# Performance work log

Hardware: AMD Instinct MI355X
Metric: run time of the kernel (lower is better)

The kernel has to match this reference:

```python
import jax, jax.numpy as jnp
import numpy as np

# Model dims (match init_kwargs)
E, D, H, K = 8, 512, 1024, 2   # num_experts, input/output dim, hidden dim, top_k
B, S = 4, 2048                 # batch, seq_len


def setup_inputs() -> dict:
    key = jax.random.key(0)
    ks = jax.random.split(key, 5)
    sd = lambda fan: np.float32(1.0 / np.sqrt(fan))
    return {
        "x": jax.random.normal(ks[0], (B, S, D), jnp.float32),
        "gate_w": jax.random.normal(ks[1], (D, E), jnp.float32) * sd(D),
        "gate_b": jnp.zeros((E,), jnp.float32),
        "w1": jax.random.normal(ks[2], (E, D, H), jnp.float32) * sd(D),
        "b1": jnp.zeros((E, H), jnp.float32),
        "w2": jax.random.normal(ks[3], (E, H, D), jnp.float32) * sd(H),
        "b2": jnp.zeros((E, D), jnp.float32),
    }


def reference(x, gate_w, gate_b, w1, b1, w2, b2):
    # x: [B, S, D]
    Bb, Ss, Dd = x.shape
    xf = x.reshape(-1, Dd)                              # [N, D], N = B*S

    # Router: softmax over experts, top-k, renormalize selected weights
    logits = xf @ gate_w + gate_b                        # [N, E]
    probs = jax.nn.softmax(logits, axis=-1)              # [N, E]
    top_w, top_i = jax.lax.top_k(probs, K)               # [N, K]
    top_w = top_w / top_w.sum(axis=-1, keepdims=True)

    # Per-token combine weight for each expert (0 if not routed).
    onehot = jax.nn.one_hot(top_i, E, dtype=probs.dtype)  # [N, K, E]
    combine = jnp.einsum("nke,nk->ne", onehot, top_w)     # [N, E]

    # Expert MLPs. Dropout is inactive at inference (identity).
    # h: [E, N, H]; GELU exact (torch nn.GELU default uses erf)
    h = jax.nn.gelu(jnp.einsum("nd,edh->enh", xf, w1) + b1[:, None, :],
                    approximate=False)
    y = jnp.einsum("enh,ehd->end", h, w2) + b2[:, None, :]  # [E, N, D]

    # Weighted combine: tokens not routed to expert e have combine[:, e] == 0.
    out = jnp.einsum("end,ne->nd", y, combine).reshape(Bb, Ss, Dd)
    return out, probs.reshape(Bb, Ss, E)
```

## Files before the change

kernel.cpp:

```cpp
#include <hip/hip_runtime.h>
#include <stdint.h>

#define N_TOK 8192
#define DIM   512
#define HID   1024
#define NE    8
#define NSLOT 16384
#define MAXSLOT 17408

typedef __attribute__((ext_vector_type(8))) short short8;
typedef __attribute__((ext_vector_type(4))) float f32x4;

#define W1T_OFF  0ull
#define W2T_OFF  8388608ull
#define H_OFF    16777216ull
#define Y_OFF    52428800ull
#define XBF_OFF  52428800ull
#define TOPI_OFF 70254592ull
#define TOPW_OFF 70320128ull
#define SLOT_OFF 70385664ull
#define ROWS_OFF 70451200ull
#define RW_OFF   70520832ull
#define CNT_OFF  70590464ull

__device__ __forceinline__ unsigned int f2bfu(float f) {
  union { float f; unsigned int i; } v; v.f = f;
  unsigned int u = v.i;
  return (u + 0x7FFFu + ((u >> 16) & 1u)) >> 16;
}
__device__ __forceinline__ float bf2f(unsigned int u) {
  union { unsigned int i; float f; } v; v.i = (u & 0xFFFFu) << 16; return v.f;
}
__device__ __forceinline__ float gelu_f(float x) {
  float x2 = x * x;
  float u = x * (1.59576912f + 0.07135481f * x2);
  float ez = __expf(-u);
  return x * __builtin_amdgcn_rcpf(1.0f + ez);
}
__device__ __forceinline__ void async16(void* lds, const void* g) {
  __builtin_amdgcn_global_load_lds(
      (const __attribute__((address_space(1))) unsigned int*)g,
      (__attribute__((address_space(3))) unsigned int*)lds, 16, 0, 0);
}

__global__ __launch_bounds__(256) void k_transpose(
    const float* __restrict__ w1, const float* __restrict__ w2,
    unsigned short* __restrict__ w1t, unsigned short* __restrict__ w2t) {
  __shared__ unsigned short tile[64][68];
  int b = blockIdx.x, tid = threadIdx.x;
  const float* src; unsigned short* dst; int R, C;
  if (b < 1024) { int e = b >> 7; int t = b & 127;
    src = w1 + (size_t)e * 524288; dst = w1t + (size_t)e * 524288; R = 512; C = 1024;
    int tr = t >> 4, tc = t & 15;
    src += (size_t)tr * 64 * C + tc * 64; dst += (size_t)tc * 64 * R + tr * 64;
  } else { b -= 1024; int e = b >> 7; int t = b & 127;
    src = w2 + (size_t)e * 524288; dst = w2t + (size_t)e * 524288; R = 1024; C = 512;
    int tr = t >> 3, tc = t & 7;
    src += (size_t)tr * 64 * C + tc * 64; dst += (size_t)tc * 64 * R + tr * 64;
  }
#pragma unroll
  for (int i = 0; i < 4; ++i) {
    int l = i * 256 + tid;
    int r = l >> 4, c4 = (l & 15) << 2;
    float4 v = *(const float4*)(src + (size_t)r * C + c4);
    tile[r][c4 + 0] = (unsigned short)f2bfu(v.x);
    tile[r][c4 + 1] = (unsigned short)f2bfu(v.y);
    tile[r][c4 + 2] = (unsigned short)f2bfu(v.z);
    tile[r][c4 + 3] = (unsigned short)f2bfu(v.w);
  }
  __syncthreads();
#pragma unroll
  for (int i = 0; i < 4; ++i) {
    int l = i * 256 + tid;
    int rr = l >> 4, c4 = (l & 15) << 2;
    ushort4 v;
    v.x = tile[c4 + 0][rr]; v.y = tile[c4 + 1][rr]; v.z = tile[c4 + 2][rr]; v.w = tile[c4 + 3][rr];
    *(ushort4*)(dst + (size_t)rr * R + c4) = v;
  }
}

__global__ __launch_bounds__(256) void k_router(
    const float* __restrict__ x, const float* __restrict__ gw,
    const float* __restrict__ gb, float* __restrict__ probs_out,
    int2* __restrict__ topi, float2* __restrict__ topw,
    unsigned short* __restrict__ xbf) {
  int wave = threadIdx.x >> 6, lane = threadIdx.x & 63;
  int n = blockIdx.x * 4 + wave;
  const float4* xr = (const float4*)(x + (size_t)n * DIM);
  float4 x0 = xr[lane * 2], x1 = xr[lane * 2 + 1];
  float xf[8] = {x0.x, x0.y, x0.z, x0.w, x1.x, x1.y, x1.z, x1.w};
  uint4 pa;
  pa.x = f2bfu(xf[0]) | (f2bfu(xf[1]) << 16);
  pa.y = f2bfu(xf[2]) | (f2bfu(xf[3]) << 16);
  pa.z = f2bfu(xf[4]) | (f2bfu(xf[5]) << 16);
  pa.w = f2bfu(xf[6]) | (f2bfu(xf[7]) << 16);
  *(uint4*)(xbf + (size_t)n * DIM + lane * 8) = pa;
  float acc[8] = {0.f,0.f,0.f,0.f,0.f,0.f,0.f,0.f};
  const float4* gwr = (const float4*)gw;
#pragma unroll
  for (int j = 0; j < 8; ++j) {
    int d = lane * 8 + j;
    float4 g0 = gwr[d * 2], g1 = gwr[d * 2 + 1];
    acc[0] += xf[j] * g0.x; acc[1] += xf[j] * g0.y; acc[2] += xf[j] * g0.z; acc[3] += xf[j] * g0.w;
    acc[4] += xf[j] * g1.x; acc[5] += xf[j] * g1.y; acc[6] += xf[j] * g1.z; acc[7] += xf[j] * g1.w;
  }
#pragma unroll
  for (int o = 1; o < 64; o <<= 1)
#pragma unroll
    for (int e = 0; e < 8; ++e) acc[e] += __shfl_xor(acc[e], o, 64);
  float p[8], mx = -1e30f, s = 0.f;
#pragma unroll
  for (int e = 0; e < 8; ++e) { p[e] = acc[e] + gb[e]; mx = fmaxf(mx, p[e]); }
#pragma unroll
  for (int e = 0; e < 8; ++e) { p[e] = __expf(p[e] - mx); s += p[e]; }
  float inv = 1.f / s;
#pragma unroll
  for (int e = 0; e < 8; ++e) p[e] *= inv;
  if (lane < 8) probs_out[(size_t)n * NE + lane] = p[lane];
  if (lane == 0) {
    int i0 = 0; float v0 = p[0];
#pragma unroll
    for (int e = 1; e < 8; ++e) if (p[e] > v0) { v0 = p[e]; i0 = e; }
    int i1 = -1; float v1 = -1.f;
#pragma unroll
    for (int e = 0; e < 8; ++e) if (e != i0 && p[e] > v1) { v1 = p[e]; i1 = e; }
    float sw = 1.f / (v0 + v1);
    topi[n] = make_int2(i0, i1);
    topw[n] = make_float2(v0 * sw, v1 * sw);
  }
}

__global__ __launch_bounds__(1024) void k_count(
    const int2* __restrict__ topi, int* __restrict__ meta, int* __restrict__ chunk_base,
    int* __restrict__ rows, float* __restrict__ rw) {
  __shared__ int ch[32][8];
  __shared__ int tot[8], poff_s[9], tiles_s[8];
  int t = threadIdx.x;
  int g = t >> 5;
  if (t < 256) ((int*)ch)[t] = 0;
  __syncthreads();
  int c[8] = {0,0,0,0,0,0,0,0};
  int base_tok = t * 8;
#pragma unroll
  for (int i = 0; i < 8; ++i) {
    int2 e = topi[base_tok + i];
#pragma unroll
    for (int k = 0; k < 8; ++k) c[k] += (e.x == k) + (e.y == k);
  }
#pragma unroll
  for (int k = 0; k < 8; ++k) if (c[k]) atomicAdd(&ch[g][k], c[k]);
  __syncthreads();
  if (t < 8) {
    int a = 0;
#pragma unroll
    for (int b = 0; b < 32; ++b) { int v = ch[b][t]; ch[b][t] = a; a += v; }
    tot[t] = a; meta[t] = a;
  }
  __syncthreads();
  if (t == 0) {
    int a = 0, ts = 0;
#pragma unroll
    for (int e = 0; e < 8; ++e) {
      int tiles = (tot[e] + 127) >> 7;
      poff_s[e] = a; tiles_s[e] = tiles;
      meta[16 + e] = a; meta[32 + e] = ts;
      a += tiles << 7; ts += tiles;
    }
    poff_s[8] = a; meta[24] = a; meta[40] = ts;
  }
  __syncthreads();
  if (t < 256) {
    int b = t >> 3, e = t & 7;
    chunk_base[t] = poff_s[e] + ch[b][e];
  }
#pragma unroll
  for (int e = 0; e < 8; ++e) {
    int padn = (tiles_s[e] << 7) - tot[e];
    if (t < padn) {
      int s = poff_s[e] + tot[e] + t;
      rows[s] = 0; rw[s] = 0.f;
    }
  }
}

__global__ __launch_bounds__(256) void k_assign(
    const int2* __restrict__ topi, const float2* __restrict__ topw,
    const int* __restrict__ chunk_base,
    int* __restrict__ rows, float* __restrict__ rw, int* __restrict__ slot_of) {
  __shared__ int lcnt[8];
  __shared__ int lbase[8];
  int t = threadIdx.x, b = blockIdx.x;
  if (t < 8) { lcnt[t] = 0; lbase[t] = chunk_base[b * 8 + t]; }
  __syncthreads();
  int n = b * 256 + t;
  int2 ei = topi[n]; float2 wv = topw[n];
  int r0 = atomicAdd(&lcnt[ei.x], 1);
  int r1 = atomicAdd(&lcnt[ei.y], 1);
  int s0 = lbase[ei.x] + r0;
  int s1 = lbase[ei.y] + r1;
  rows[s0] = n; rw[s0] = wv.x; slot_of[2 * n] = s0;
  rows[s1] = n; rw[s1] = wv.y; slot_of[2 * n + 1] = s1;
}

__global__ __launch_bounds__(256) void k_gemm1(
    const unsigned short* __restrict__ xbf, const unsigned short* __restrict__ w1t,
    const float* __restrict__ b1, const int* __restrict__ meta,
    const int* __restrict__ rows, unsigned short* __restrict__ h) {
  int t = blockIdx.y;
  if (t >= meta[40]) return;
  int e = 0;
#pragma unroll
  for (int i = 1; i < 8; ++i) if (t >= meta[32 + i]) e = i;
  int mt = t - meta[32 + e];
  int row0 = meta[16 + e] + (mt << 7);
  int nt = blockIdx.x;
  __shared__ __align__(16) unsigned short As[2][8192];
  __shared__ __align__(16) unsigned short Bs[2][8192];
  int tid = threadIdx.x;
  int wave = tid >> 6, lane = tid & 63;
  int wr = wave & 1, wc = wave >> 1;
  f32x4 acc[4][4] = {};
  const unsigned short* bBase = w1t + (size_t)e * HID * DIM + (size_t)(nt * 128) * DIM;

  const unsigned short* ga[4]; const unsigned short* gb[4];
#pragma unroll
  for (int j = 0; j < 4; ++j) {
    int s = j * 256 + tid;
    int r = s >> 3;
    int cg = ((s & 7) ^ (r & 7)) << 3;
    ga[j] = xbf + (size_t)rows[row0 + r] * DIM + cg;
    gb[j] = bBase + (size_t)r * DIM + cg;
  }
  int ldst = (wave * 64) * 8;

#pragma unroll
  for (int j = 0; j < 4; ++j) {
    async16(&As[0][j * 2048 + ldst], ga[j]);
    async16(&Bs[0][j * 2048 + ldst], gb[j]);
  }
  __syncthreads();

  for (int k0 = 0; k0 < DIM; k0 += 64) {
    int cur = (k0 >> 6) & 1, nxt = cur ^ 1;
    if (k0 + 64 < DIM) {
#pragma unroll
      for (int j = 0; j < 4; ++j) {
        async16(&As[nxt][j * 2048 + ldst], ga[j] + k0 + 64);
        async16(&Bs[nxt][j * 2048 + ldst], gb[j] + k0 + 64);
      }
    }
#pragma unroll
    for (int kk = 0; kk < 2; ++kk) {
      int ca = kk * 4 + (lane >> 4);
      short8 tf[4], wf[4];
#pragma unroll
      for (int am = 0; am < 4; ++am) {
        int ra = wr * 64 + am * 16 + (lane & 15);
        tf[am] = *(const short8*)&As[cur][(ra * 8 + (ca ^ (ra & 7))) * 8];
      }
#pragma unroll
      for (int an = 0; an < 4; ++an) {
        int rb = wc * 64 + an * 16 + (lane & 15);
        wf[an] = *(const short8*)&Bs[cur][(rb * 8 + (ca ^ (rb & 7))) * 8];
      }
#pragma unroll
      for (int an = 0; an < 4; ++an)
#pragma unroll
        for (int am = 0; am < 4; ++am)
          acc[an][am] = __builtin_amdgcn_mfma_f32_16x16x32_bf16(wf[an], tf[am], acc[an][am], 0, 0, 0);
    }
    __syncthreads();
  }
  int ml = lane & 15, q = lane >> 4;
#pragma unroll
  for (int am = 0; am < 4; ++am) {
    int slot_r = row0 + wr * 64 + am * 16 + ml;
    unsigned short* hrow = h + (size_t)slot_r * HID;
#pragma unroll
    for (int an = 0; an < 4; ++an) {
      int colb = nt * 128 + wc * 64 + an * 16 + q * 4;
      float4 bias = *(const float4*)&b1[e * HID + colb];
      f32x4 v = acc[an][am];
      float g0 = gelu_f(v[0] + bias.x);
      float g1 = gelu_f(v[1] + bias.y);
      float g2 = gelu_f(v[2] + bias.z);
      float g3 = gelu_f(v[3] + bias.w);
      uint2 pk;
      pk.x = f2bfu(g0) | (f2bfu(g1) << 16);
      pk.y = f2bfu(g2) | (f2bfu(g3) << 16);
      *(uint2*)(hrow + colb) = pk;
    }
  }
}

__global__ __launch_bounds__(256) void k_gemm2(
    const unsigned short* __restrict__ h, const unsigned short* __restrict__ w2t,
    const float* __restrict__ b2, const int* __restrict__ meta,
    const float* __restrict__ rw, unsigned short* __restrict__ y) {
  int t = blockIdx.y;
  if (t >= meta[40]) return;
  int e = 0;
#pragma unroll
  for (int i = 1; i < 8; ++i) if (t >= meta[32 + i]) e = i;
  int mt = t - meta[32 + e];
  int row0 = meta[16 + e] + (mt << 7);
  int nt = blockIdx.x;
  __shared__ __align__(16) unsigned short As[2][8192];
  __shared__ __align__(16) unsigned short Bs[2][8192];
  int tid = threadIdx.x;
  int wave = tid >> 6, lane = tid & 63;
  int wr = wave & 1, wc = wave >> 1;
  f32x4 acc[4][4] = {};
  const unsigned short* aBase = h + (size_t)row0 * HID;
  const unsigned short* bBase = w2t + (size_t)e * DIM * HID + (size_t)(nt * 128) * HID;

  const unsigned short* ga[4]; const unsigned short* gb[4];
#pragma unroll
  for (int j = 0; j < 4; ++j) {
    int s = j * 256 + tid;
    int r = s >> 3;
    int cg = ((s & 7) ^ (r & 7)) << 3;
    ga[j] = aBase + (size_t)r * HID + cg;
    gb[j] = bBase + (size_t)r * HID + cg;
  }
  int ldst = (wave * 64) * 8;

#pragma unroll
  for (int j = 0; j < 4; ++j) {
    async16(&As[0][j * 2048 + ldst], ga[j]);
    async16(&Bs[0][j * 2048 + ldst], gb[j]);
  }
  __syncthreads();

  for (int k0 = 0; k0 < HID; k0 += 64) {
    int cur = (k0 >> 6) & 1, nxt = cur ^ 1;
    if (k0 + 64 < HID) {
#pragma unroll
      for (int j = 0; j < 4; ++j) {
        async16(&As[nxt][j * 2048 + ldst], ga[j] + k0 + 64);
        async16(&Bs[nxt][j * 2048 + ldst], gb[j] + k0 + 64);
      }
    }
#pragma unroll
    for (int kk = 0; kk < 2; ++kk) {
      int ca = kk * 4 + (lane >> 4);
      short8 tf[4], wf[4];
#pragma unroll
      for (int am = 0; am < 4; ++am) {
        int ra = wr * 64 + am * 16 + (lane & 15);
        tf[am] = *(const short8*)&As[cur][(ra * 8 + (ca ^ (ra & 7))) * 8];
      }
#pragma unroll
      for (int an = 0; an < 4; ++an) {
        int rb = wc * 64 + an * 16 + (lane & 15);
        wf[an] = *(const short8*)&Bs[cur][(rb * 8 + (ca ^ (rb & 7))) * 8];
      }
#pragma unroll
      for (int an = 0; an < 4; ++an)
#pragma unroll
        for (int am = 0; am < 4; ++am)
          acc[an][am] = __builtin_amdgcn_mfma_f32_16x16x32_bf16(wf[an], tf[am], acc[an][am], 0, 0, 0);
    }
    __syncthreads();
  }
  int ml = lane & 15, q = lane >> 4;
#pragma unroll
  for (int am = 0; am < 4; ++am) {
    int slot_r = row0 + wr * 64 + am * 16 + ml;
    float w = rw[slot_r];
    unsigned short* yrow = y + (size_t)slot_r * DIM;
#pragma unroll
    for (int an = 0; an < 4; ++an) {
      int colb = nt * 128 + wc * 64 + an * 16 + q * 4;
      float4 bias = *(const float4*)&b2[e * DIM + colb];
      f32x4 v = acc[an][am];
      uint2 pk;
      pk.x = f2bfu((v[0] + bias.x) * w) | (f2bfu((v[1] + bias.y) * w) << 16);
      pk.y = f2bfu((v[2] + bias.z) * w) | (f2bfu((v[3] + bias.w) * w) << 16);
      *(uint2*)(yrow + colb) = pk;
    }
  }
}

__global__ __launch_bounds__(256) void k_combine(
    const unsigned short* __restrict__ y, const int* __restrict__ slot_of,
    float* __restrict__ out) {
  int t = blockIdx.x * 256 + threadIdx.x;
  int n = t >> 6, c = (t & 63) << 3;
  int s0 = slot_of[2 * n], s1 = slot_of[2 * n + 1];
  uint4 u0 = *(const uint4*)(y + (size_t)s0 * DIM + c);
  uint4 u1 = *(const uint4*)(y + (size_t)s1 * DIM + c);
  float4 o0, o1;
  o0.x = bf2f(u0.x) + bf2f(u1.x); o0.y = bf2f(u0.x >> 16) + bf2f(u1.x >> 16);
  o0.z = bf2f(u0.y) + bf2f(u1.y); o0.w = bf2f(u0.y >> 16) + bf2f(u1.y >> 16);
  o1.x = bf2f(u0.z) + bf2f(u1.z); o1.y = bf2f(u0.z >> 16) + bf2f(u1.z >> 16);
  o1.z = bf2f(u0.w) + bf2f(u1.w); o1.w = bf2f(u0.w >> 16) + bf2f(u1.w >> 16);
  *(float4*)(out + (size_t)n * DIM + c) = o0;
  *(float4*)(out + (size_t)n * DIM + c + 4) = o1;
}

extern "C" void kernel_launch(void* const* d_in, const int* in_sizes, int n_in,
                              void* d_out, int out_size, void* d_ws, size_t ws_size,
                              hipStream_t stream) {
  const float* x  = (const float*)d_in[0];
  const float* gw = (const float*)d_in[1];
  const float* gb = (const float*)d_in[2];
  const float* w1 = (const float*)d_in[3];
  const float* b1 = (const float*)d_in[4];
  const float* w2 = (const float*)d_in[5];
  const float* b2 = (const float*)d_in[6];
  float* out = (float*)d_out;
  char* ws = (char*)d_ws;

  unsigned short* w1t = (unsigned short*)(ws + W1T_OFF);
  unsigned short* w2t = (unsigned short*)(ws + W2T_OFF);
  unsigned short* h   = (unsigned short*)(ws + H_OFF);
  unsigned short* y   = (unsigned short*)(ws + Y_OFF);
  unsigned short* xbf = (unsigned short*)(ws + XBF_OFF);
  int2*   topi    = (int2*)(ws + TOPI_OFF);
  float2* topw    = (float2*)(ws + TOPW_OFF);
  int*    slot_of = (int*)(ws + SLOT_OFF);
  int*    rows    = (int*)(ws + ROWS_OFF);
  float*  rw      = (float*)(ws + RW_OFF);
  int*    meta    = (int*)(ws + CNT_OFF);
  int*    chunk_base = meta + 64;
  float*  probs   = out + (size_t)N_TOK * DIM;

  k_transpose<<<dim3(2048), dim3(256), 0, stream>>>(w1, w2, w1t, w2t);
  k_router   <<<dim3(2048), dim3(256), 0, stream>>>(x, gw, gb, probs, topi, topw, xbf);
  k_count    <<<dim3(1),    dim3(1024), 0, stream>>>(topi, meta, chunk_base, rows, rw);
  k_assign   <<<dim3(32),   dim3(256), 0, stream>>>(topi, topw, chunk_base, rows, rw, slot_of);
  k_gemm1    <<<dim3(8, 136), dim3(256), 0, stream>>>(xbf, w1t, b1, meta, rows, h);
  k_gemm2    <<<dim3(4, 136), dim3(256), 0, stream>>>(h, w2t, b2, meta, rw, y);
  k_combine  <<<dim3(2048), dim3(256), 0, stream>>>(y, slot_of, out);
}
```

Before: 214.2 us.

## Stage GEMM tile prefetch through registers instead of direct global-to-LDS loads

Both expert GEMM kernels stop using the direct global-to-LDS async load for tiles. They now load the next tile into registers (uint4) before the MFMA loop and write those registers into the other LDS buffer afterwards, followed by a barrier. A sched_barrier keeps the compiler from moving the LDS stores ahead of the compute. The goal is to overlap global memory latency with MFMA work under explicit control. The cost is extra VGPR pressure and extra LDS store instructions, which could reduce occupancy.

Result: slower. 327.9 us (+53.1%).

```diff
diff --git a/kernel.cpp b/kernel.cpp
--- a/kernel.cpp
+++ b/kernel.cpp
@@ -36,11 +36,6 @@
   float u = x * (1.59576912f + 0.07135481f * x2);
   float ez = __expf(-u);
   return x * __builtin_amdgcn_rcpf(1.0f + ez);
-}
-__device__ __forceinline__ void async16(void* lds, const void* g) {
-  __builtin_amdgcn_global_load_lds(
-      (const __attribute__((address_space(1))) unsigned int*)g,
-      (__attribute__((address_space(3))) unsigned int*)lds, 16, 0, 0);
 }
 
 __global__ __launch_bounds__(256) void k_transpose(
@@ -222,7 +217,7 @@
   f32x4 acc[4][4] = {};
   const unsigned short* bBase = w1t + (size_t)e * HID * DIM + (size_t)(nt * 128) * DIM;
 
-  const unsigned short* ga[4]; const unsigned short* gb[4];
+  const unsigned short* ga[4]; const unsigned short* gb[4]; int lofs[4];
 #pragma unroll
   for (int j = 0; j < 4; ++j) {
     int s = j * 256 + tid;
@@ -230,23 +225,27 @@
     int cg = ((s & 7) ^ (r & 7)) << 3;
     ga[j] = xbf + (size_t)rows[row0 + r] * DIM + cg;
     gb[j] = bBase + (size_t)r * DIM + cg;
-  }
-  int ldst = (wave * 64) * 8;
-
+    lofs[j] = s * 8;
+  }
+
+  uint4 pa[4], pb[4];
+#pragma unroll
+  for (int j = 0; j < 4; ++j) { pa[j] = *(const uint4*)ga[j]; pb[j] = *(const uint4*)gb[j]; }
 #pragma unroll
   for (int j = 0; j < 4; ++j) {
-    async16(&As[0][j * 2048 + ldst], ga[j]);
-    async16(&Bs[0][j * 2048 + ldst], gb[j]);
+    *(uint4*)&As[0][lofs[j]] = pa[j];
+    *(uint4*)&Bs[0][lofs[j]] = pb[j];
   }
   __syncthreads();
 
   for (int k0 = 0; k0 < DIM; k0 += 64) {
     int cur = (k0 >> 6) & 1, nxt = cur ^ 1;
-    if (k0 + 64 < DIM) {
+    bool more = (k0 + 64 < DIM);
+    if (more) {
 #pragma unroll
       for (int j = 0; j < 4; ++j) {
-        async16(&As[nxt][j * 2048 + ldst], ga[j] + k0 + 64);
-        async16(&Bs[nxt][j * 2048 + ldst], gb[j] + k0 + 64);
+        pa[j] = *(const uint4*)(ga[j] + k0 + 64);
+        pb[j] = *(const uint4*)(gb[j] + k0 + 64);
       }
     }
 #pragma unroll
@@ -269,7 +268,15 @@
         for (int am = 0; am < 4; ++am)
           acc[an][am] = __builtin_amdgcn_mfma_f32_16x16x32_bf16(wf[an], tf[am], acc[an][am], 0, 0, 0);
     }
-    __syncthreads();
+    __builtin_amdgcn_sched_barrier(0);
+    if (more) {
+#pragma unroll
+      for (int j = 0; j < 4; ++j) {
+        *(uint4*)&As[nxt][lofs[j]] = pa[j];
+        *(uint4*)&Bs[nxt][lofs[j]] = pb[j];
+      }
+      __syncthreads();
+    }
   }
   int ml = lane & 15, q = lane >> 4;
 #pragma unroll
@@ -314,7 +321,7 @@
   const unsigned short* aBase = h + (size_t)row0 * HID;
   const unsigned short* bBase = w2t + (size_t)e * DIM * HID + (size_t)(nt * 128) * HID;
 
-  const unsigned short* ga[4]; const unsigned short* gb[4];
+  const unsigned short* ga[4]; const unsigned short* gb[4]; int lofs[4];
 #pragma unroll
   for (int j = 0; j < 4; ++j) {
     int s = j * 256 + tid;
@@ -322,23 +329,27 @@
     int cg = ((s & 7) ^ (r & 7)) << 3;
     ga[j] = aBase + (size_t)r * HID + cg;
     gb[j] = bBase + (size_t)r * HID + cg;
-  }
-  int ldst = (wave * 64) * 8;
-
+    lofs[j] = s * 8;
+  }
+
+  uint4 pa[4], pb[4];
+#pragma unroll
+  for (int j = 0; j < 4; ++j) { pa[j] = *(const uint4*)ga[j]; pb[j] = *(const uint4*)gb[j]; }
 #pragma unroll
   for (int j = 0; j < 4; ++j) {
-    async16(&As[0][j * 2048 + ldst], ga[j]);
-    async16(&Bs[0][j * 2048 + ldst], gb[j]);
+    *(uint4*)&As[0][lofs[j]] = pa[j];
+    *(uint4*)&Bs[0][lofs[j]] = pb[j];
   }
   __syncthreads();
 
   for (int k0 = 0; k0 < HID; k0 += 64) {
     int cur = (k0 >> 6) & 1, nxt = cur ^ 1;
-    if (k0 + 64 < HID) {
+    bool more = (k0 + 64 < HID);
+    if (more) {
 #pragma unroll
       for (int j = 0; j < 4; ++j) {
-        async16(&As[nxt][j * 2048 + ldst], ga[j] + k0 + 64);
-        async16(&Bs[nxt][j * 2048 + ldst], gb[j] + k0 + 64);
+        pa[j] = *(const uint4*)(ga[j] + k0 + 64);
+        pb[j] = *(const uint4*)(gb[j] + k0 + 64);
       }
     }
 #pragma unroll
@@ -361,7 +372,15 @@
         for (int am = 0; am < 4; ++am)
           acc[an][am] = __builtin_amdgcn_mfma_f32_16x16x32_bf16(wf[an], tf[am], acc[an][am], 0, 0, 0);
     }
-    __syncthreads();
+    __builtin_amdgcn_sched_barrier(0);
+    if (more) {
+#pragma unroll
+      for (int j = 0; j < 4; ++j) {
+        *(uint4*)&As[nxt][lofs[j]] = pa[j];
+        *(uint4*)&Bs[nxt][lofs[j]] = pb[j];
+      }
+      __syncthreads();
+    }
   }
   int ml = lane & 15, q = lane >> 4;
 #pragma unroll
```

## Halve GEMM K-tile to 32 with new LDS swizzle; widen transpose stores

Applied to the files above, without the earlier changes.

Both expert GEMM kernels now stage 32-wide K slices instead of 64, which halves shared memory per block (64KB to 32KB) and uses a 4-chunk XOR swizzle keyed on row pairs. The goal is higher occupancy, with more blocks resident per CU to hide latency. The cost is twice as many loop iterations and barriers, with less MFMA work per sync. The weight-transpose kernel also switches from 8-byte to 16-byte global stores.

Result: no change. 210.4 us (-1.8%).

```diff
diff --git a/kernel.cpp b/kernel.cpp
--- a/kernel.cpp
+++ b/kernel.cpp
@@ -70,12 +70,20 @@
   }
   __syncthreads();
 #pragma unroll
-  for (int i = 0; i < 4; ++i) {
+  for (int i = 0; i < 2; ++i) {
     int l = i * 256 + tid;
-    int rr = l >> 4, c4 = (l & 15) << 2;
-    ushort4 v;
-    v.x = tile[c4 + 0][rr]; v.y = tile[c4 + 1][rr]; v.z = tile[c4 + 2][rr]; v.w = tile[c4 + 3][rr];
-    *(ushort4*)(dst + (size_t)rr * R + c4) = v;
+    int rr = l >> 3, c8 = (l & 7) << 3;
+    ushort4 a, b2v;
+    a.x = tile[c8 + 0][rr]; a.y = tile[c8 + 1][rr];
+    a.z = tile[c8 + 2][rr]; a.w = tile[c8 + 3][rr];
+    b2v.x = tile[c8 + 4][rr]; b2v.y = tile[c8 + 5][rr];
+    b2v.z = tile[c8 + 6][rr]; b2v.w = tile[c8 + 7][rr];
+    uint4 pk;
+    pk.x = (unsigned int)a.x | ((unsigned int)a.y << 16);
+    pk.y = (unsigned int)a.z | ((unsigned int)a.w << 16);
+    pk.z = (unsigned int)b2v.x | ((unsigned int)b2v.y << 16);
+    pk.w = (unsigned int)b2v.z | ((unsigned int)b2v.w << 16);
+    *(uint4*)(dst + (size_t)rr * R + c8) = pk;
   }
 }
 
@@ -214,54 +222,53 @@
   int mt = t - meta[32 + e];
   int row0 = meta[16 + e] + (mt << 7);
   int nt = blockIdx.x;
-  __shared__ __align__(16) unsigned short As[2][8192];
-  __shared__ __align__(16) unsigned short Bs[2][8192];
+  __shared__ __align__(16) unsigned short As[2][4096];
+  __shared__ __align__(16) unsigned short Bs[2][4096];
   int tid = threadIdx.x;
   int wave = tid >> 6, lane = tid & 63;
   int wr = wave & 1, wc = wave >> 1;
   f32x4 acc[4][4] = {};
   const unsigned short* bBase = w1t + (size_t)e * HID * DIM + (size_t)(nt * 128) * DIM;
 
-  const unsigned short* ga[4]; const unsigned short* gb[4];
-#pragma unroll
-  for (int j = 0; j < 4; ++j) {
+  const unsigned short* ga[2]; const unsigned short* gb[2];
+#pragma unroll
+  for (int j = 0; j < 2; ++j) {
     int s = j * 256 + tid;
-    int r = s >> 3;
-    int cg = ((s & 7) ^ (r & 7)) << 3;
+    int r = s >> 2;
+    int cg = ((s & 3) ^ ((r >> 1) & 3)) << 3;
     ga[j] = xbf + (size_t)rows[row0 + r] * DIM + cg;
     gb[j] = bBase + (size_t)r * DIM + cg;
   }
   int ldst = (wave * 64) * 8;
 
 #pragma unroll
-  for (int j = 0; j < 4; ++j) {
+  for (int j = 0; j < 2; ++j) {
     async16(&As[0][j * 2048 + ldst], ga[j]);
     async16(&Bs[0][j * 2048 + ldst], gb[j]);
   }
   __syncthreads();
 
-  for (int k0 = 0; k0 < DIM; k0 += 64) {
-    int cur = (k0 >> 6) & 1, nxt = cur ^ 1;
-    if (k0 + 64 < DIM) {
-#pragma unroll
-      for (int j = 0; j < 4; ++j) {
-        async16(&As[nxt][j * 2048 + ldst], ga[j] + k0 + 64);
-        async16(&Bs[nxt][j * 2048 + ldst], gb[j] + k0 + 64);
-      }
-    }
-#pragma unroll
-    for (int kk = 0; kk < 2; ++kk) {
-      int ca = kk * 4 + (lane >> 4);
+  for (int k0 = 0; k0 < DIM; k0 += 32) {
+    int cur = (k0 >> 5) & 1, nxt = cur ^ 1;
+    if (k0 + 32 < DIM) {
+#pragma unroll
+      for (int j = 0; j < 2; ++j) {
+        async16(&As[nxt][j * 2048 + ldst], ga[j] + k0 + 32);
+        async16(&Bs[nxt][j * 2048 + ldst], gb[j] + k0 + 32);
+      }
+    }
+    {
+      int ca = lane >> 4;
       short8 tf[4], wf[4];
 #pragma unroll
       for (int am = 0; am < 4; ++am) {
         int ra = wr * 64 + am * 16 + (lane & 15);
-        tf[am] = *(const short8*)&As[cur][(ra * 8 + (ca ^ (ra & 7))) * 8];
+        tf[am] = *(const short8*)&As[cur][(ra * 4 + (ca ^ ((ra >> 1) & 3))) * 8];
       }
 #pragma unroll
       for (int an = 0; an < 4; ++an) {
         int rb = wc * 64 + an * 16 + (lane & 15);
-        wf[an] = *(const short8*)&Bs[cur][(rb * 8 + (ca ^ (rb & 7))) * 8];
+        wf[an] = *(const short8*)&Bs[cur][(rb * 4 + (ca ^ ((rb >> 1) & 3))) * 8];
       }
 #pragma unroll
       for (int an = 0; an < 4; ++an)
@@ -305,8 +312,8 @@
   int mt = t - meta[32 + e];
   int row0 = meta[16 + e] + (mt << 7);
   int nt = blockIdx.x;
-  __shared__ __align__(16) unsigned short As[2][8192];
-  __shared__ __align__(16) unsigned short Bs[2][8192];
+  __shared__ __align__(16) unsigned short As[2][4096];
+  __shared__ __align__(16) unsigned short Bs[2][4096];
   int tid = threadIdx.x;
   int wave = tid >> 6, lane = tid & 63;
   int wr = wave & 1, wc = wave >> 1;
@@ -314,46 +321,45 @@
   const unsigned short* aBase = h + (size_t)row0 * HID;
   const unsigned short* bBase = w2t + (size_t)e * DIM * HID + (size_t)(nt * 128) * HID;
 
-  const unsigned short* ga[4]; const unsigned short* gb[4];
-#pragma unroll
-  for (int j = 0; j < 4; ++j) {
+  const unsigned short* ga[2]; const unsigned short* gb[2];
+#pragma unroll
+  for (int j = 0; j < 2; ++j) {
     int s = j * 256 + tid;
-    int r = s >> 3;
-    int cg = ((s & 7) ^ (r & 7)) << 3;
+    int r = s >> 2;
+    int cg = ((s & 3) ^ ((r >> 1) & 3)) << 3;
     ga[j] = aBase + (size_t)r * HID + cg;
     gb[j] = bBase + (size_t)r * HID + cg;
   }
   int ldst = (wave * 64) * 8;
 
 #pragma unroll
-  for (int j = 0; j < 4; ++j) {
+  for (int j = 0; j < 2; ++j) {
     async16(&As[0][j * 2048 + ldst], ga[j]);
     async16(&Bs[0][j * 2048 + ldst], gb[j]);
   }
   __syncthreads();
 
-  for (int k0 = 0; k0 < HID; k0 += 64) {
-    int cur = (k0 >> 6) & 1, nxt = cur ^ 1;
-    if (k0 + 64 < HID) {
-#pragma unroll
-      for (int j = 0; j < 4; ++j) {
-        async16(&As[nxt][j * 2048 + ldst], ga[j] + k0 + 64);
-        async16(&Bs[nxt][j * 2048 + ldst], gb[j] + k0 + 64);
-      }
-    }
-#pragma unroll
-    for (int kk = 0; kk < 2; ++kk) {
-      int ca = kk * 4 + (lane >> 4);
+  for (int k0 = 0; k0 < HID; k0 += 32) {
+    int cur = (k0 >> 5) & 1, nxt = cur ^ 1;
+    if (k0 + 32 < HID) {
+#pragma unroll
+      for (int j = 0; j < 2; ++j) {
+        async16(&As[nxt][j * 2048 + ldst], ga[j] + k0 + 32);
+        async16(&Bs[nxt][j * 2048 + ldst], gb[j] + k0 + 32);
+      }
+    }
+    {
+      int ca = lane >> 4;
       short8 tf[4], wf[4];
 #pragma unroll
       for (int am = 0; am < 4; ++am) {
         int ra = wr * 64 + am * 16 + (lane & 15);
-        tf[am] = *(const short8*)&As[cur][(ra * 8 + (ca ^ (ra & 7))) * 8];
+        tf[am] = *(const short8*)&As[cur][(ra * 4 + (ca ^ ((ra >> 1) & 3))) * 8];
       }
 #pragma unroll
       for (int an = 0; an < 4; ++an) {
         int rb = wc * 64 + an * 16 + (lane & 15);
-        wf[an] = *(const short8*)&Bs[cur][(rb * 8 + (ca ^ (rb & 7))) * 8];
+        wf[an] = *(const short8*)&Bs[cur][(rb * 4 + (ca ^ ((rb >> 1) & 3))) * 8];
       }
 #pragma unroll
       for (int an = 0; an < 4; ++an)
```

## Fuse transpose with router, widen transpose stores, halve gemm2 N tile

Applied to the files above, without the earlier changes.

The weight transpose/bf16 conversion and the router are merged into one launch with 4096 blocks, removing a kernel boundary and letting the two independent jobs overlap. The transpose write-back now stores 8 bf16 values (16 bytes) per thread instead of 4. gemm2 switches from 128x128 tiles to 128x64 tiles, with each wave owning 32 rows by 64 columns, which doubles the grid to 8x136 for more parallelism. The cost is more A-tile reloads in gemm2 and less MFMA work per LDS read.

New measurement: 219.7 us. +2.6%, slower.

```diff
diff --git a/kernel.cpp b/kernel.cpp
--- a/kernel.cpp
+++ b/kernel.cpp
@@ -43,11 +43,62 @@
       (__attribute__((address_space(3))) unsigned int*)lds, 16, 0, 0);
 }
 
-__global__ __launch_bounds__(256) void k_transpose(
+__global__ __launch_bounds__(256) void k_prep(
     const float* __restrict__ w1, const float* __restrict__ w2,
-    unsigned short* __restrict__ w1t, unsigned short* __restrict__ w2t) {
+    unsigned short* __restrict__ w1t, unsigned short* __restrict__ w2t,
+    const float* __restrict__ x, const float* __restrict__ gw,
+    const float* __restrict__ gb, float* __restrict__ probs_out,
+    int2* __restrict__ topi, float2* __restrict__ topw,
+    unsigned short* __restrict__ xbf) {
   __shared__ unsigned short tile[64][68];
   int b = blockIdx.x, tid = threadIdx.x;
+  if (b >= 2048) {
+    int wave = tid >> 6, lane = tid & 63;
+    int n = (b - 2048) * 4 + wave;
+    const float4* xr = (const float4*)(x + (size_t)n * DIM);
+    float4 x0 = xr[lane * 2], x1 = xr[lane * 2 + 1];
+    float xf[8] = {x0.x, x0.y, x0.z, x0.w, x1.x, x1.y, x1.z, x1.w};
+    uint4 pa;
+    pa.x = f2bfu(xf[0]) | (f2bfu(xf[1]) << 16);
+    pa.y = f2bfu(xf[2]) | (f2bfu(xf[3]) << 16);
+    pa.z = f2bfu(xf[4]) | (f2bfu(xf[5]) << 16);
+    pa.w = f2bfu(xf[6]) | (f2bfu(xf[7]) << 16);
+    *(uint4*)(xbf + (size_t)n * DIM + lane * 8) = pa;
+    float acc[8] = {0.f,0.f,0.f,0.f,0.f,0.f,0.f,0.f};
+    const float4* gwr = (const float4*)gw;
+#pragma unroll
+    for (int j = 0; j < 8; ++j) {
+      int d = lane * 8 + j;
+      float4 g0 = gwr[d * 2], g1 = gwr[d * 2 + 1];
+      acc[0] += xf[j] * g0.x; acc[1] += xf[j] * g0.y; acc[2] += xf[j] * g0.z; acc[3] += xf[j] * g0.w;
+      acc[4] += xf[j] * g1.x; acc[5] += xf[j] * g1.y; acc[6] += xf[j] * g1.z; acc[7] += xf[j] * g1.w;
+    }
+#pragma unroll
+    for (int o = 1; o < 64; o <<= 1)
+#pragma unroll
+      for (int e = 0; e < 8; ++e) acc[e] += __shfl_xor(acc[e], o, 64);
+    float p[8], mx = -1e30f, s = 0.f;
+#pragma unroll
+    for (int e = 0; e < 8; ++e) { p[e] = acc[e] + gb[e]; mx = fmaxf(mx, p[e]); }
+#pragma unroll
+    for (int e = 0; e < 8; ++e) { p[e] = __expf(p[e] - mx); s += p[e]; }
+    float inv = 1.f / s;
+#pragma unroll
+    for (int e = 0; e < 8; ++e) p[e] *= inv;
+    if (lane < 8) probs_out[(size_t)n * NE + lane] = p[lane];
+    if (lane == 0) {
+      int i0 = 0; float v0 = p[0];
+#pragma unroll
+      for (int e = 1; e < 8; ++e) if (p[e] > v0) { v0 = p[e]; i0 = e; }
+      int i1 = -1; float v1 = -1.f;
+#pragma unroll
+      for (int e = 0; e < 8; ++e) if (e != i0 && p[e] > v1) { v1 = p[e]; i1 = e; }
+      float sw = 1.f / (v0 + v1);
+      topi[n] = make_int2(i0, i1);
+      topw[n] = make_float2(v0 * sw, v1 * sw);
+    }
+    return;
+  }
   const float* src; unsigned short* dst; int R, C;
   if (b < 1024) { int e = b >> 7; int t = b & 127;
     src = w1 + (size_t)e * 524288; dst = w1t + (size_t)e * 524288; R = 512; C = 1024;
@@ -70,63 +121,20 @@
   }
   __syncthreads();
 #pragma unroll
-  for (int i = 0; i < 4; ++i) {
+  for (int i = 0; i < 2; ++i) {
     int l = i * 256 + tid;
-    int rr = l >> 4, c4 = (l & 15) << 2;
-    ushort4 v;
-    v.x = tile[c4 + 0][rr]; v.y = tile[c4 + 1][rr]; v.z = tile[c4 + 2][rr]; v.w = tile[c4 + 3][rr];
-    *(ushort4*)(dst + (size_t)rr * R + c4) = v;
-  }
-}
-
-__global__ __launch_bounds__(256) void k_router(
-    const float* __restrict__ x, const float* __restrict__ gw,
-    const float* __restrict__ gb, float* __restrict__ probs_out,
-    int2* __restrict__ topi, float2* __restrict__ topw,
-    unsigned short* __restrict__ xbf) {
-  int wave = threadIdx.x >> 6, lane = threadIdx.x & 63;
-  int n = blockIdx.x * 4 + wave;
-  const float4* xr = (const float4*)(x + (size_t)n * DIM);
-  float4 x0 = xr[lane * 2], x1 = xr[lane * 2 + 1];
-  float xf[8] = {x0.x, x0.y, x0.z, x0.w, x1.x, x1.y, x1.z, x1.w};
-  uint4 pa;
-  pa.x = f2bfu(xf[0]) | (f2bfu(xf[1]) << 16);
-  pa.y = f2bfu(xf[2]) | (f2bfu(xf[3]) << 16);
-  pa.z = f2bfu(xf[4]) | (f2bfu(xf[5]) << 16);
-  pa.w = f2bfu(xf[6]) | (f2bfu(xf[7]) << 16);
-  *(uint4*)(xbf + (size_t)n * DIM + lane * 8) = pa;
-  float acc[8] = {0.f,0.f,0.f,0.f,0.f,0.f,0.f,0.f};
-  const float4* gwr = (const float4*)gw;
-#pragma unroll
-  for (int j = 0; j < 8; ++j) {
-    int d = lane * 8 + j;
-    float4 g0 = gwr[d * 2], g1 = gwr[d * 2 + 1];
-    acc[0] += xf[j] * g0.x; acc[1] += xf[j] * g0.y; acc[2] += xf[j] * g0.z; acc[3] += xf[j] * g0.w;
-    acc[4] += xf[j] * g1.x; acc[5] += xf[j] * g1.y; acc[6] += xf[j] * g1.z; acc[7] += xf[j] * g1.w;
-  }
-#pragma unroll
-  for (int o = 1; o < 64; o <<= 1)
-#pragma unroll
-    for (int e = 0; e < 8; ++e) acc[e] += __shfl_xor(acc[e], o, 64);
-  float p[8], mx = -1e30f, s = 0.f;
-#pragma unroll
-  for (int e = 0; e < 8; ++e) { p[e] = acc[e] + gb[e]; mx = fmaxf(mx, p[e]); }
-#pragma unroll
-  for (int e = 0; e < 8; ++e) { p[e] = __expf(p[e] - mx); s += p[e]; }
-  float inv = 1.f / s;
-#pragma unroll
-  for (int e = 0; e < 8; ++e) p[e] *= inv;
-  if (lane < 8) probs_out[(size_t)n * NE + lane] = p[lane];
-  if (lane == 0) {
-    int i0 = 0; float v0 = p[0];
-#pragma unroll
-    for (int e = 1; e < 8; ++e) if (p[e] > v0) { v0 = p[e]; i0 = e; }
-    int i1 = -1; float v1 = -1.f;
-#pragma unroll
-    for (int e = 0; e < 8; ++e) if (e != i0 && p[e] > v1) { v1 = p[e]; i1 = e; }
-    float sw = 1.f / (v0 + v1);
-    topi[n] = make_int2(i0, i1);
-    topw[n] = make_float2(v0 * sw, v1 * sw);
+    int rr = l >> 3, c8 = (l & 7) << 3;
+    ushort4 a, b2v;
+    a.x = tile[c8 + 0][rr]; a.y = tile[c8 + 1][rr];
+    a.z = tile[c8 + 2][rr]; a.w = tile[c8 + 3][rr];
+    b2v.x = tile[c8 + 4][rr]; b2v.y = tile[c8 + 5][rr];
+    b2v.z = tile[c8 + 6][rr]; b2v.w = tile[c8 + 7][rr];
+    uint4 pk;
+    pk.x = (unsigned int)a.x | ((unsigned int)a.y << 16);
+    pk.y = (unsigned int)a.z | ((unsigned int)a.w << 16);
+    pk.z = (unsigned int)b2v.x | ((unsigned int)b2v.y << 16);
+    pk.w = (unsigned int)b2v.z | ((unsigned int)b2v.w << 16);
+    *(uint4*)(dst + (size_t)rr * R + c8) = pk;
   }
 }
 
@@ -306,72 +314,75 @@
   int row0 = meta[16 + e] + (mt << 7);
   int nt = blockIdx.x;
   __shared__ __align__(16) unsigned short As[2][8192];
-  __shared__ __align__(16) unsigned short Bs[2][8192];
+  __shared__ __align__(16) unsigned short Bs[2][4096];
   int tid = threadIdx.x;
   int wave = tid >> 6, lane = tid & 63;
-  int wr = wave & 1, wc = wave >> 1;
-  f32x4 acc[4][4] = {};
+  f32x4 acc[4][2] = {};
   const unsigned short* aBase = h + (size_t)row0 * HID;
-  const unsigned short* bBase = w2t + (size_t)e * DIM * HID + (size_t)(nt * 128) * HID;
-
-  const unsigned short* ga[4]; const unsigned short* gb[4];
+  const unsigned short* bBase = w2t + (size_t)e * DIM * HID + (size_t)(nt * 64) * HID;
+
+  const unsigned short* ga[4]; const unsigned short* gb[2];
 #pragma unroll
   for (int j = 0; j < 4; ++j) {
     int s = j * 256 + tid;
     int r = s >> 3;
     int cg = ((s & 7) ^ (r & 7)) << 3;
     ga[j] = aBase + (size_t)r * HID + cg;
+  }
+#pragma unroll
+  for (int j = 0; j < 2; ++j) {
+    int s = j * 256 + tid;
+    int r = s >> 3;
+    int cg = ((s & 7) ^ (r & 7)) << 3;
     gb[j] = bBase + (size_t)r * HID + cg;
   }
   int ldst = (wave * 64) * 8;
 
 #pragma unroll
-  for (int j = 0; j < 4; ++j) {
-    async16(&As[0][j * 2048 + ldst], ga[j]);
-    async16(&Bs[0][j * 2048 + ldst], gb[j]);
-  }
+  for (int j = 0; j < 4; ++j) async16(&As[0][j * 2048 + ldst], ga[j]);
+#pragma unroll
+  for (int j = 0; j < 2; ++j) async16(&Bs[0][j * 2048 + ldst], gb[j]);
   __syncthreads();
 
   for (int k0 = 0; k0 < HID; k0 += 64) {
     int cur = (k0 >> 6) & 1, nxt = cur ^ 1;
     if (k0 + 64 < HID) {
 #pragma unroll
-      for (int j = 0; j < 4; ++j) {
-        async16(&As[nxt][j * 2048 + ldst], ga[j] + k0 + 64);
-        async16(&Bs[nxt][j * 2048 + ldst], gb[j] + k0 + 64);
-      }
+      for (int j = 0; j < 4; ++j) async16(&As[nxt][j * 2048 + ldst], ga[j] + k0 + 64);
+#pragma unroll
+      for (int j = 0; j < 2; ++j) async16(&Bs[nxt][j * 2048 + ldst], gb[j] + k0 + 64);
     }
 #pragma unroll
     for (int kk = 0; kk < 2; ++kk) {
       int ca = kk * 4 + (lane >> 4);
-      short8 tf[4], wf[4];
-#pragma unroll
-      for (int am = 0; am < 4; ++am) {
-        int ra = wr * 64 + am * 16 + (lane & 15);
+      short8 tf[2], wf[4];
+#pragma unroll
+      for (int am = 0; am < 2; ++am) {
+        int ra = wave * 32 + am * 16 + (lane & 15);
         tf[am] = *(const short8*)&As[cur][(ra * 8 + (ca ^ (ra & 7))) * 8];
       }
 #pragma unroll
       for (int an = 0; an < 4; ++an) {
-        int rb = wc * 64 + an * 16 + (lane & 15);
+        int rb = an * 16 + (lane & 15);
         wf[an] = *(const short8*)&Bs[cur][(rb * 8 + (ca ^ (rb & 7))) * 8];
       }
 #pragma unroll
       for (int an = 0; an < 4; ++an)
 #pragma unroll
-        for (int am = 0; am < 4; ++am)
+        for (int am = 0; am < 2; ++am)
           acc[an][am] = __builtin_amdgcn_mfma_f32_16x16x32_bf16(wf[an], tf[am], acc[an][am], 0, 0, 0);
     }
     __syncthreads();
   }
   int ml = lane & 15, q = lane >> 4;
 #pragma unroll
-  for (int am = 0; am < 4; ++am) {
-    int slot_r = row0 + wr * 64 + am * 16 + ml;
+  for (int am = 0; am < 2; ++am) {
+    int slot_r = row0 + wave * 32 + am * 16 + ml;
     float w = rw[slot_r];
     unsigned short* yrow = y + (size_t)slot_r * DIM;
 #pragma unroll
     for (int an = 0; an < 4; ++an) {
-      int colb = nt * 128 + wc * 64 + an * 16 + q * 4;
+      int colb = nt * 64 + an * 16 + q * 4;
       float4 bias = *(const float4*)&b2[e * DIM + colb];
       f32x4 v = acc[an][am];
       uint2 pk;
@@ -426,11 +437,11 @@
   int*    chunk_base = meta + 64;
   float*  probs   = out + (size_t)N_TOK * DIM;
 
-  k_transpose<<<dim3(2048), dim3(256), 0, stream>>>(w1, w2, w1t, w2t);
-  k_router   <<<dim3(2048), dim3(256), 0, stream>>>(x, gw, gb, probs, topi, topw, xbf);
-  k_count    <<<dim3(1),    dim3(1024), 0, stream>>>(topi, meta, chunk_base, rows, rw);
-  k_assign   <<<dim3(32),   dim3(256), 0, stream>>>(topi, topw, chunk_base, rows, rw, slot_of);
-  k_gemm1    <<<dim3(8, 136), dim3(256), 0, stream>>>(xbf, w1t, b1, meta, rows, h);
-  k_gemm2    <<<dim3(4, 136), dim3(256), 0, stream>>>(h, w2t, b2, meta, rw, y);
-  k_combine  <<<dim3(2048), dim3(256), 0, stream>>>(y, slot_of, out);
-}
+  k_prep   <<<dim3(4096), dim3(256), 0, stream>>>(w1, w2, w1t, w2t,
+                                                  x, gw, gb, probs, topi, topw, xbf);
+  k_count  <<<dim3(1),    dim3(1024), 0, stream>>>(topi, meta, chunk_base, rows, rw);
+  k_assign <<<dim3(32),   dim3(256), 0, stream>>>(topi, topw, chunk_base, rows, rw, slot_of);
+  k_gemm1  <<<dim3(8, 136), dim3(256), 0, stream>>>(xbf, w1t, b1, meta, rows, h);
+  k_gemm2  <<<dim3(8, 136), dim3(256), 0, stream>>>(h, w2t, b2, meta, rw, y);
+  k_combine<<<dim3(2048), dim3(256), 0, stream>>>(y, slot_of, out);
+}
```
